# Performance work log

Hardware: AMD Instinct MI355X
Metric: run time of the kernel (lower is better)

The kernel has to match this reference:

```python
import jax, jax.numpy as jnp
import numpy as np

N_NODES = 50000
N_EDGES = 1600000
N_GRAPHS = 512
HEADS = 4
HEAD_DIM = 32
LAYERS = 3
NEG_SLOPE = 0.2


def setup_inputs() -> dict:
    key = jax.random.key(0)
    ks = jax.random.split(key, 7)
    x = jax.random.normal(ks[0], (N_NODES, 128), dtype=jnp.float32)
    Ws = jax.random.normal(ks[1], (LAYERS, 128, 128), dtype=jnp.float32) * 0.1
    att_src = jax.random.normal(ks[2], (LAYERS, HEADS, HEAD_DIM), dtype=jnp.float32) * 0.1
    att_dst = jax.random.normal(ks[3], (LAYERS, HEADS, HEAD_DIM), dtype=jnp.float32) * 0.1
    biases = jnp.zeros((LAYERS, 128), dtype=jnp.float32)
    edge_index = jax.random.randint(ks[4], (2, N_EDGES), 0, N_NODES, dtype=jnp.int64)
    batch = jnp.sort(jax.random.randint(ks[5], (N_NODES,), 0, N_GRAPHS, dtype=jnp.int64))
    return {"x": x, "Ws": Ws, "att_src": att_src, "att_dst": att_dst,
            "biases": biases, "edge_index": edge_index, "batch": batch}


def _gat_layer(x, W, a_s, a_d, b, src, dst, n):
    # linear transform -> per-head features [N, H, C]
    h = (x @ W).reshape(n, HEADS, HEAD_DIM)
    # per-node attention halves [N, H]
    alpha_src = jnp.einsum('nhc,hc->nh', h, a_s)
    alpha_dst = jnp.einsum('nhc,hc->nh', h, a_d)
    # edge logits [E, H]
    e = jax.nn.leaky_relu(alpha_src[src] + alpha_dst[dst], NEG_SLOPE)
    # segment softmax over incoming edges of each destination node
    m = jax.ops.segment_max(e, dst, num_segments=n)
    w = jnp.exp(e - m[dst])
    denom = jax.ops.segment_sum(w, dst, num_segments=n)
    alpha = w / (denom[dst] + 1e-16)
    # weighted scatter-add of source features [E, H, C] -> [N, H, C]
    msg = h[src] * alpha[:, :, None]
    out = jax.ops.segment_sum(msg, dst, num_segments=n)
    return out.reshape(n, HEADS * HEAD_DIM) + b


def reference(x, Ws, att_src, att_dst, biases, edge_index, batch):
    n = x.shape[0]
    # PyG GATConv adds self-loops by default
    loops = jnp.arange(n, dtype=edge_index.dtype)
    src = jnp.concatenate([edge_index[0], loops])
    dst = jnp.concatenate([edge_index[1], loops])
    for l in range(LAYERS):
        x = jax.nn.elu(_gat_layer(x, Ws[l], att_src[l], att_dst[l], biases[l], src, dst, n))
        # dropout is identity in eval mode
    # global mean pool over graphs
    sums = jax.ops.segment_sum(x, batch, num_segments=N_GRAPHS)
    cnt = jax.ops.segment_sum(jnp.ones((n,), x.dtype), batch, num_segments=N_GRAPHS)
    return sums / jnp.maximum(cnt, 1.0)[:, None]
```

## Files before the change

### kernel.cpp

```cpp
#include <hip/hip_runtime.h>
#include <hip/hip_fp16.h>
#include <math.h>

#define HEADS 4
#define HDIM 32
#define FD 128
#define NEG 0.2f
#define BCAP 4608
#define CH 8192
#define CHW 128

typedef _Float16 f16x8 __attribute__((ext_vector_type(8)));
typedef float f32x4 __attribute__((ext_vector_type(4)));

__device__ __forceinline__ float lrelu(float x) { return fmaxf(x, NEG * x); }

__global__ __launch_bounds__(256) void k_prep(const float* __restrict__ x,
                                              __half* __restrict__ o, long nF,
                                              const float* __restrict__ W,
                                              const float* __restrict__ att_s,
                                              const float* __restrict__ att_d,
                                              _Float16* __restrict__ W16T,
                                              float* __restrict__ va_s,
                                              float* __restrict__ va_d,
                                              int* __restrict__ bcnt, int nbuck,
                                              int ncvt) {
    int b = blockIdx.x;
    if (b < ncvt) {
        long i = ((long)b * 256 + threadIdx.x) * 4;
        if (i < nF) {
            float4 v = *(const float4*)&x[i];
            *(__half2*)&o[i] = __floats2half2_rn(v.x, v.y);
            *(__half2*)&o[i + 2] = __floats2half2_rn(v.z, v.w);
        }
        return;
    }
    if (b == ncvt + 3) {
        for (int i = threadIdx.x; i < nbuck; i += 256) bcnt[i] = 0;
        return;
    }
    int l = b - ncvt;
    const float* Wl = W + (long)l * FD * FD;
    _Float16* ow = W16T + (long)l * FD * FD;
    for (int i = threadIdx.x; i < FD * FD; i += 256) {
        int k = i >> 7, n = i & 127;
        ow[n * FD + k] = (_Float16)Wl[i];
    }
    const float* as_l = att_s + l * HEADS * HDIM;
    const float* ad_l = att_d + l * HEADS * HDIM;
    for (int idx = threadIdx.x; idx < HEADS * FD; idx += 256) {
        int hd = idx >> 7, k = idx & 127;
        float ss = 0.f, dd = 0.f;
        for (int c = 0; c < HDIM; ++c) {
            float w = Wl[k * FD + hd * HDIM + c];
            ss += w * as_l[hd * HDIM + c];
            dd += w * ad_l[hd * HDIM + c];
        }
        va_s[(long)l * HEADS * FD + idx] = ss;
        va_d[(long)l * HEADS * FD + idx] = dd;
    }
}

__global__ __launch_bounds__(256) void k_gemm_mfma(const __half* __restrict__ x16,
                                                   const _Float16* __restrict__ W16T,
                                                   __half* __restrict__ h, int N) {
    __shared__ _Float16 wl[FD * FD];
    int t = threadIdx.x;
    for (int i = t * 8; i < FD * FD; i += 2048)
        *(f16x8*)&wl[i] = *(const f16x8*)&W16T[i];

    int w = t >> 6, lane = t & 63;
    int m = lane & 15, quad = lane >> 4;
    int row0 = blockIdx.x * 128 + w * 32;

    f16x8 a[2][4];
    f16x8 zf = {};
#pragma unroll
    for (int rt = 0; rt < 2; ++rt) {
        int gr = row0 + rt * 16 + m;
#pragma unroll
        for (int kc = 0; kc < 4; ++kc)
            a[rt][kc] = (gr < N) ? *(const f16x8*)&x16[(long)gr * FD + kc * 32 + quad * 8] : zf;
    }
    f32x4 acc[2][8];
#pragma unroll
    for (int rt = 0; rt < 2; ++rt)
#pragma unroll
        for (int c = 0; c < 8; ++c) acc[rt][c] = (f32x4){0.f, 0.f, 0.f, 0.f};

    __syncthreads();
#pragma unroll
    for (int c = 0; c < 8; ++c) {
        int nb = c * 16 + m;
#pragma unroll
        for (int kc = 0; kc < 4; ++kc) {
            f16x8 b = *(f16x8*)&wl[nb * FD + kc * 32 + quad * 8];
            acc[0][c] = __builtin_amdgcn_mfma_f32_16x16x32_f16(a[0][kc], b, acc[0][c], 0, 0, 0);
            acc[1][c] = __builtin_amdgcn_mfma_f32_16x16x32_f16(a[1][kc], b, acc[1][c], 0, 0, 0);
        }
    }
#pragma unroll
    for (int rt = 0; rt < 2; ++rt) {
        int rbase = row0 + rt * 16 + quad * 4;
#pragma unroll
        for (int c = 0; c < 8; ++c) {
            int col = c * 16 + m;
#pragma unroll
            for (int i = 0; i < 4; ++i) {
                int gr = rbase + i;
                if (gr < N) h[(long)gr * FD + col] = __float2half(acc[rt][c][i]);
            }
        }
    }
}

__global__ __launch_bounds__(256) void k_alpha(const __half* __restrict__ h,
                                               const float* __restrict__ a_s,
                                               const float* __restrict__ a_d,
                                               float* __restrict__ as_o,
                                               float* __restrict__ ad_o, int N) {
    int t = threadIdx.x;
    int n = blockIdx.x * 16 + (t >> 4);
    if (n >= N) return;
    int c16 = t & 15, gh = c16 >> 2, cb = c16 * 8;
    int c32 = (c16 & 3) * 8;
    float4 raw = *(const float4*)&h[(long)n * FD + cb];
    const __half* hh = (const __half*)&raw;
    float vs = 0.f, vd = 0.f;
#pragma unroll
    for (int i = 0; i < 8; ++i) {
        float hv = __half2float(hh[i]);
        vs += hv * a_s[gh * HDIM + c32 + i];
        vd += hv * a_d[gh * HDIM + c32 + i];
    }
    vs += __shfl_xor(vs, 1); vs += __shfl_xor(vs, 2);
    vd += __shfl_xor(vd, 1); vd += __shfl_xor(vd, 2);
    if ((c16 & 3) == 0) {
        as_o[n * HEADS + gh] = vs;
        ad_o[n * HEADS + gh] = vd;
    }
}

__global__ __launch_bounds__(1024) void k_bin(const int* __restrict__ ei, int NE,
                                              int nbuck,
                                              int* __restrict__ bcnt,
                                              int* __restrict__ binned) {
    __shared__ int hist[512];
    __shared__ int gbase[512];
    int t = threadIdx.x;
    int c0 = blockIdx.x * CH;
    if (t < 512) hist[t] = 0;
    __syncthreads();
    int sub[8], val[8], loff[8];
#pragma unroll
    for (int k = 0; k < 8; ++k) {
        int idx = c0 + k * 1024 + t;
        sub[k] = -1;
        if (idx < NE) {
            int s = ei[idx], d = ei[NE + idx];
            sub[k] = d >> 7;
            val[k] = s | ((d & 127) << 16);
            loff[k] = atomicAdd(&hist[sub[k]], 1);
        }
    }
    __syncthreads();
    if (t < 512 && t < nbuck && hist[t] > 0)
        gbase[t] = atomicAdd(&bcnt[t], hist[t]);
    __syncthreads();
#pragma unroll
    for (int k = 0; k < 8; ++k) {
        if (sub[k] >= 0) {
            int p = gbase[sub[k]] + loff[k];
            if (p < BCAP) binned[(long)sub[k] * BCAP + p] = val[k];
        }
    }
}

__global__ __launch_bounds__(1024) void k_scan_sub(const int* __restrict__ bcnt,
                                                   int* __restrict__ bbase, int n,
                                                   int* __restrict__ rowstart, int N, int NE,
                                                   float* __restrict__ cnt, int G,
                                                   float* __restrict__ outz) {
    __shared__ int sm[1024];
    int t = threadIdx.x;
    int c0 = t * 4;
    int v0 = (c0 < n) ? bcnt[c0] : 0;
    int v1 = (c0 + 1 < n) ? bcnt[c0 + 1] : 0;
    int v2 = (c0 + 2 < n) ? bcnt[c0 + 2] : 0;
    int v3 = (c0 + 3 < n) ? bcnt[c0 + 3] : 0;
    int tot = v0 + v1 + v2 + v3;
    sm[t] = tot;
    if (t < G) cnt[t] = 0.f;
    __syncthreads();
    for (int off = 1; off < 1024; off <<= 1) {
        int u = (t >= off) ? sm[t - off] : 0;
        __syncthreads();
        sm[t] += u;
        __syncthreads();
    }
    int base = sm[t] - tot;
    if (c0 < n) bbase[c0] = base;
    if (c0 + 1 < n) bbase[c0 + 1] = base + v0;
    if (c0 + 2 < n) bbase[c0 + 2] = base + v0 + v1;
    if (c0 + 3 < n) bbase[c0 + 3] = base + v0 + v1 + v2;
    if (t == 1023) {
        bbase[n] = sm[1023];
        rowstart[N] = NE;
    }
    long tot_out = (long)G * FD;
    for (long i = t * 4; i < tot_out; i += 4096)
        *(float4*)&outz[i] = (float4){0.f, 0.f, 0.f, 0.f};
}

__global__ __launch_bounds__(256) void k_bucket_csr(const int* __restrict__ binned,
                                                    const int* __restrict__ bcnt,
                                                    const int* __restrict__ bbase,
                                                    int* __restrict__ csr_src,
                                                    int* __restrict__ rowstart, int N) {
    int b = blockIdx.x;
    int t = threadIdx.x;
    __shared__ int ldeg[128], lofs[128], lcur[128];
    __shared__ int lcsr[BCAP];
    if (t < 128) ldeg[t] = 0;
    __syncthreads();
    int cnt = bcnt[b];
    if (cnt > BCAP) cnt = BCAP;
    int base = bbase[b];
    const int* reg = binned + (long)b * BCAP;
    for (int i = t; i < cnt; i += 256)
        atomicAdd(&ldeg[reg[i] >> 16], 1);
    __syncthreads();
    if (t < 128) lofs[t] = ldeg[t];
    __syncthreads();
    for (int off = 1; off < 128; off <<= 1) {
        int u = (t < 128 && t >= off) ? lofs[t - off] : 0;
        __syncthreads();
        if (t < 128) lofs[t] += u;
        __syncthreads();
    }
    if (t < 128) lcur[t] = lofs[t] - ldeg[t];
    __syncthreads();
    for (int i = t; i < cnt; i += 256) {
        int v = reg[i];
        int p = atomicAdd(&lcur[v >> 16], 1);
        lcsr[p] = v & 0xFFFF;
    }
    __syncthreads();
    for (int i = t; i < cnt; i += 256) csr_src[base + i] = lcsr[i];
    if (t < 128) {
        int d = b * 128 + t;
        if (d < N) rowstart[d] = base + lofs[t] - ldeg[t];
    }
}

__global__ __launch_bounds__(256) void k_aggr(const int* __restrict__ csr_src,
                                              const int* __restrict__ rowstart,
                                              const float* __restrict__ as_,
                                              const float* __restrict__ ad_,
                                              const __half* __restrict__ h,
                                              const float* __restrict__ bias,
                                              const float* __restrict__ va_s,
                                              const float* __restrict__ va_d,
                                              float* __restrict__ as_n,
                                              float* __restrict__ ad_n,
                                              __half* __restrict__ out, int N) {
    __shared__ int s_all[4][CHW];
    int t = threadIdx.x;
    int wv = t >> 6, lane = t & 63;
    int n = blockIdx.x * 4 + wv;
    if (n >= N) return;
    int* s_lds = s_all[wv];
    int c16 = lane & 15, rg = lane >> 4;
    int gh = c16 >> 2;
    int cb = c16 * 8;
    int beg = rowstart[n], end = rowstart[n + 1];
    int deg = end - beg;
    float adn = ad_[n * HEADS + gh];
    float l = 0.f;
    float acc[8] = {0.f, 0.f, 0.f, 0.f, 0.f, 0.f, 0.f, 0.f};

    for (int c0 = 0; c0 < deg; c0 += CHW) {
        int cnt = deg - c0;
        if (cnt > CHW) cnt = CHW;
        for (int i = lane; i < cnt; i += 64) s_lds[i] = csr_src[beg + c0 + i] << 2;
        __builtin_amdgcn_wave_barrier();
#pragma unroll 2
        for (int e = rg; e < cnt; e += 4) {
            int s4 = s_lds[e];
            float lg = lrelu(as_[s4 + gh] + adn);
            float w = __expf(fminf(lg, 30.f));
            l += w;
            float4 raw = *(const float4*)&h[((long)s4 << 5) + cb];
            const __half* hh = (const __half*)&raw;
#pragma unroll
            for (int i = 0; i < 8; ++i)
                acc[i] += __half2float(hh[i]) * w;
        }
        __builtin_amdgcn_wave_barrier();
    }
    l += __shfl_xor(l, 16);
    l += __shfl_xor(l, 32);
#pragma unroll
    for (int i = 0; i < 8; ++i) {
        acc[i] += __shfl_xor(acc[i], 16);
        acc[i] += __shfl_xor(acc[i], 32);
    }
    float sl = lrelu(as_[n * HEADS + gh] + adn);
    float sw = __expf(fminf(sl, 30.f));
    float inv = 1.f / (l + sw + 1e-16f);
    float4 rawh = *(const float4*)&h[(long)n * FD + cb];
    const __half* hh = (const __half*)&rawh;
    float4 b0 = *(const float4*)&bias[cb];
    float4 b1 = *(const float4*)&bias[cb + 4];
    float bb[8] = {b0.x, b0.y, b0.z, b0.w, b1.x, b1.y, b1.z, b1.w};
    float v[8];
#pragma unroll
    for (int i = 0; i < 8; ++i) {
        float u = (acc[i] + sw * __half2float(hh[i])) * inv + bb[i];
        v[i] = u > 0.f ? u : __expf(u) - 1.f;
    }
    if (rg == 0) {
        __half o8[8];
#pragma unroll
        for (int i = 0; i < 8; ++i) o8[i] = __float2half(v[i]);
        *(float4*)&out[(long)n * FD + cb] = *(float4*)o8;
    }
    if (va_s) {
        const float* vs = va_s + rg * FD + cb;
        const float* vd = va_d + rg * FD + cb;
        float ps = 0.f, pd = 0.f;
#pragma unroll
        for (int i = 0; i < 8; ++i) {
            ps += v[i] * vs[i];
            pd += v[i] * vd[i];
        }
        for (int off = 1; off < 16; off <<= 1) {
            ps += __shfl_xor(ps, off);
            pd += __shfl_xor(pd, off);
        }
        if (c16 == 0) {
            as_n[n * HEADS + rg] = ps;
            ad_n[n * HEADS + rg] = pd;
        }
    }
}

__global__ __launch_bounds__(128) void k_pool(const __half* __restrict__ x,
                                              const int* __restrict__ batch,
                                              float* __restrict__ out,
                                              float* __restrict__ cnt, int N) {
    int n0 = blockIdx.x * 32;
    if (n0 >= N) return;
    int n1 = n0 + 32;
    if (n1 > N) n1 = N;
    int ch = threadIdx.x;
    __shared__ int gb[32];
    if (ch < n1 - n0) gb[ch] = batch[n0 + ch];
    __syncthreads();
    int g = gb[0];
    float sum = 0.f, c_local = 0.f;
    for (int n = n0; n < n1; ++n) {
        int gn = gb[n - n0];
        if (gn != g) {
            atomicAdd(&out[(long)g * FD + ch], sum);
            if (ch == 0) atomicAdd(&cnt[g], c_local);
            sum = 0.f;
            c_local = 0.f;
            g = gn;
        }
        sum += __half2float(x[(long)n * FD + ch]);
        c_local += 1.f;
    }
    atomicAdd(&out[(long)g * FD + ch], sum);
    if (ch == 0) atomicAdd(&cnt[g], c_local);
}

__global__ void k_div(float* __restrict__ out, const float* __restrict__ cnt, int G) {
    int i = blockIdx.x * 256 + threadIdx.x;
    if (i >= G * FD) return;
    float c = cnt[i >> 7];
    out[i] /= (c > 1.f ? c : 1.f);
}

extern "C" void kernel_launch(void* const* d_in, const int* in_sizes, int n_in,
                              void* d_out, int out_size, void* d_ws, size_t ws_size,
                              hipStream_t stream) {
    const float* x0     = (const float*)d_in[0];
    const float* Wall   = (const float*)d_in[1];
    const float* att_s  = (const float*)d_in[2];
    const float* att_d  = (const float*)d_in[3];
    const float* biases = (const float*)d_in[4];
    const int*   ei     = (const int*)d_in[5];
    const int*   batch  = (const int*)d_in[6];
    float*       out    = (float*)d_out;

    int N  = in_sizes[0] / FD;
    int NE = in_sizes[5] / 2;
    int G  = out_size / FD;

    int nbuck = (N + 127) >> 7;

    long nF = (long)N * FD;
    float*    wsf      = (float*)d_ws;
    float*    asA      = wsf;
    float*    adA      = asA + (long)N * HEADS;
    float*    asB      = adA + (long)N * HEADS;
    float*    adB      = asB + (long)N * HEADS;
    float*    cnt      = adB + (long)N * HEADS;
    float*    va_s     = cnt + G;
    float*    va_d     = va_s + 3 * HEADS * FD;
    int*      rowstart = (int*)(va_d + 3 * HEADS * FD);
    int*      bcnt     = rowstart + N + 1;
    int*      bbase    = bcnt + nbuck;
    int*      csr_src  = bbase + nbuck + 1;
    __half*   h        = (__half*)(csr_src + NE);
    __half*   x16      = h + nF;
    _Float16* W16T     = (_Float16*)(x16 + nF);
    int*      binned   = (int*)(W16T + 3 * FD * FD);

    int ncvt = (int)((nF / 4 + 255) / 256);

    k_prep<<<ncvt + 4, 256, 0, stream>>>(x0, x16, nF, Wall, att_s, att_d,
                                         W16T, va_s, va_d, bcnt, nbuck, ncvt);
    k_bin<<<(NE + CH - 1) / CH, 1024, 0, stream>>>(ei, NE, nbuck, bcnt, binned);
    k_scan_sub<<<1, 1024, 0, stream>>>(bcnt, bbase, nbuck, rowstart, N, NE, cnt, G, out);
    k_bucket_csr<<<nbuck, 256, 0, stream>>>(binned, bcnt, bbase, csr_src, rowstart, N);

    float* asR[3] = {asA, asB, asA};
    float* adR[3] = {adA, adB, adA};
    for (int l = 0; l < 3; ++l) {
        k_gemm_mfma<<<(N + 127) / 128, 256, 0, stream>>>(x16, W16T + (long)l * FD * FD, h, N);
        if (l == 0)
            k_alpha<<<(N + 15) / 16, 256, 0, stream>>>(h, att_s, att_d, asA, adA, N);
        const float* vs = (l < 2) ? va_s + (long)(l + 1) * HEADS * FD : nullptr;
        const float* vd = (l < 2) ? va_d + (long)(l + 1) * HEADS * FD : nullptr;
        k_aggr<<<(N + 3) / 4, 256, 0, stream>>>(csr_src, rowstart, asR[l], adR[l], h,
                                                biases + l * FD, vs, vd,
                                                asR[l + 1 < 3 ? l + 1 : 0],
                                                adR[l + 1 < 3 ? l + 1 : 0], x16, N);
    }

    k_pool<<<(N + 31) / 32, 128, 0, stream>>>(x16, batch, out, cnt, N);
    k_div<<<(G * FD + 255) / 256, 256, 0, stream>>>(out, cnt, G);
}
```

Before: 356.4 us.

## Split GAT aggregation per head with 16-bit CSR indices and per-layer alpha kernel

Rewrites the aggregation kernel so each block handles one head for 16 nodes, with 16 lanes per node gathering 32-channel head slices over 4 edges at a time. Blocks are ordered so that all four heads of neighbouring node groups run close together, which should help reuse of gathered rows in L2. CSR source indices are stored as 16-bit values, and the LDS index staging is removed. The fused next-layer attention projection is dropped and k_alpha runs every layer instead, which adds a kernel launch and an extra read of h per layer in exchange for a lighter aggregation epilogue. The 16-bit indices only work while the node count stays below 65536.

```diff
diff --git a/kernel.cpp b/kernel.cpp
--- a/kernel.cpp
+++ b/kernel.cpp
@@ -8,7 +8,6 @@
 #define NEG 0.2f
 #define BCAP 4608
 #define CH 8192
-#define CHW 128
 
 typedef _Float16 f16x8 __attribute__((ext_vector_type(8)));
 typedef float f32x4 __attribute__((ext_vector_type(4)));
@@ -18,11 +17,7 @@
 __global__ __launch_bounds__(256) void k_prep(const float* __restrict__ x,
                                               __half* __restrict__ o, long nF,
                                               const float* __restrict__ W,
-                                              const float* __restrict__ att_s,
-                                              const float* __restrict__ att_d,
                                               _Float16* __restrict__ W16T,
-                                              float* __restrict__ va_s,
-                                              float* __restrict__ va_d,
                                               int* __restrict__ bcnt, int nbuck,
                                               int ncvt) {
     int b = blockIdx.x;
@@ -46,19 +41,6 @@
         int k = i >> 7, n = i & 127;
         ow[n * FD + k] = (_Float16)Wl[i];
     }
-    const float* as_l = att_s + l * HEADS * HDIM;
-    const float* ad_l = att_d + l * HEADS * HDIM;
-    for (int idx = threadIdx.x; idx < HEADS * FD; idx += 256) {
-        int hd = idx >> 7, k = idx & 127;
-        float ss = 0.f, dd = 0.f;
-        for (int c = 0; c < HDIM; ++c) {
-            float w = Wl[k * FD + hd * HDIM + c];
-            ss += w * as_l[hd * HDIM + c];
-            dd += w * ad_l[hd * HDIM + c];
-        }
-        va_s[(long)l * HEADS * FD + idx] = ss;
-        va_d[(long)l * HEADS * FD + idx] = dd;
-    }
 }
 
 __global__ __launch_bounds__(256) void k_gemm_mfma(const __half* __restrict__ x16,
@@ -215,7 +197,7 @@
 __global__ __launch_bounds__(256) void k_bucket_csr(const int* __restrict__ binned,
                                                     const int* __restrict__ bcnt,
                                                     const int* __restrict__ bbase,
-                                                    int* __restrict__ csr_src,
+                                                    unsigned short* __restrict__ csr16,
                                                     int* __restrict__ rowstart, int N) {
     int b = blockIdx.x;
     int t = threadIdx.x;
@@ -246,102 +228,76 @@
         lcsr[p] = v & 0xFFFF;
     }
     __syncthreads();
-    for (int i = t; i < cnt; i += 256) csr_src[base + i] = lcsr[i];
+    for (int i = t; i < cnt; i += 256) csr16[base + i] = (unsigned short)lcsr[i];
     if (t < 128) {
         int d = b * 128 + t;
         if (d < N) rowstart[d] = base + lofs[t] - ldeg[t];
     }
 }
 
-__global__ __launch_bounds__(256) void k_aggr(const int* __restrict__ csr_src,
+__global__ __launch_bounds__(256) void k_aggr(const unsigned short* __restrict__ csr16,
                                               const int* __restrict__ rowstart,
                                               const float* __restrict__ as_,
                                               const float* __restrict__ ad_,
                                               const __half* __restrict__ h,
                                               const float* __restrict__ bias,
-                                              const float* __restrict__ va_s,
-                                              const float* __restrict__ va_d,
-                                              float* __restrict__ as_n,
-                                              float* __restrict__ ad_n,
                                               __half* __restrict__ out, int N) {
-    __shared__ int s_all[4][CHW];
     int t = threadIdx.x;
     int wv = t >> 6, lane = t & 63;
-    int n = blockIdx.x * 4 + wv;
-    if (n >= N) return;
-    int* s_lds = s_all[wv];
-    int c16 = lane & 15, rg = lane >> 4;
-    int gh = c16 >> 2;
-    int cb = c16 * 8;
-    int beg = rowstart[n], end = rowstart[n + 1];
-    int deg = end - beg;
-    float adn = ad_[n * HEADS + gh];
+    int b = blockIdx.x;
+    int head = (b & 7) >> 1;
+    int ng = (b >> 3) * 2 + (b & 1);
+    int m = lane >> 4;
+    int g = (lane >> 2) & 3;
+    int l4 = lane & 3;
+    int n = ng * 16 + wv * 4 + m;
+    bool nv = n < N;
+    int nc = nv ? n : 0;
+    int beg = rowstart[nc];
+    int deg = nv ? rowstart[nc + 1] - beg : 0;
+    int hofs = head * 32 + l4 * 8;
+    float adn = ad_[nc * HEADS + head];
+    float asn = as_[nc * HEADS + head];
+    float4 rawh = *(const float4*)&h[(long)nc * FD + hofs];
+    float4 b0 = *(const float4*)&bias[hofs];
+    float4 b1 = *(const float4*)&bias[hofs + 4];
+
     float l = 0.f;
     float acc[8] = {0.f, 0.f, 0.f, 0.f, 0.f, 0.f, 0.f, 0.f};
-
-    for (int c0 = 0; c0 < deg; c0 += CHW) {
-        int cnt = deg - c0;
-        if (cnt > CHW) cnt = CHW;
-        for (int i = lane; i < cnt; i += 64) s_lds[i] = csr_src[beg + c0 + i] << 2;
-        __builtin_amdgcn_wave_barrier();
-#pragma unroll 2
-        for (int e = rg; e < cnt; e += 4) {
-            int s4 = s_lds[e];
-            float lg = lrelu(as_[s4 + gh] + adn);
-            float w = __expf(fminf(lg, 30.f));
-            l += w;
-            float4 raw = *(const float4*)&h[((long)s4 << 5) + cb];
-            const __half* hh = (const __half*)&raw;
-#pragma unroll
-            for (int i = 0; i < 8; ++i)
-                acc[i] += __half2float(hh[i]) * w;
-        }
-        __builtin_amdgcn_wave_barrier();
-    }
-    l += __shfl_xor(l, 16);
-    l += __shfl_xor(l, 32);
+    for (int e0 = 0; e0 < deg; e0 += 4) {
+        int e = e0 + g;
+        int ec = e < deg ? e : deg - 1;
+        int src = (int)__builtin_nontemporal_load(&csr16[beg + ec]);
+        float a = as_[src * HEADS + head];
+        float w = __expf(fminf(lrelu(a + adn), 30.f));
+        if (e >= deg) w = 0.f;
+        l += w;
+        float4 rr = *(const float4*)&h[(long)src * FD + hofs];
+        const __half* hh = (const __half*)&rr;
+#pragma unroll
+        for (int i = 0; i < 8; ++i)
+            acc[i] += __half2float(hh[i]) * w;
+    }
+    l += __shfl_xor(l, 4);
+    l += __shfl_xor(l, 8);
 #pragma unroll
     for (int i = 0; i < 8; ++i) {
-        acc[i] += __shfl_xor(acc[i], 16);
-        acc[i] += __shfl_xor(acc[i], 32);
-    }
-    float sl = lrelu(as_[n * HEADS + gh] + adn);
-    float sw = __expf(fminf(sl, 30.f));
+        acc[i] += __shfl_xor(acc[i], 4);
+        acc[i] += __shfl_xor(acc[i], 8);
+    }
+    float sw = __expf(fminf(lrelu(asn + adn), 30.f));
     float inv = 1.f / (l + sw + 1e-16f);
-    float4 rawh = *(const float4*)&h[(long)n * FD + cb];
     const __half* hh = (const __half*)&rawh;
-    float4 b0 = *(const float4*)&bias[cb];
-    float4 b1 = *(const float4*)&bias[cb + 4];
     float bb[8] = {b0.x, b0.y, b0.z, b0.w, b1.x, b1.y, b1.z, b1.w};
-    float v[8];
-#pragma unroll
-    for (int i = 0; i < 8; ++i) {
-        float u = (acc[i] + sw * __half2float(hh[i])) * inv + bb[i];
-        v[i] = u > 0.f ? u : __expf(u) - 1.f;
-    }
-    if (rg == 0) {
+    if (g == 0 && nv) {
         __half o8[8];
 #pragma unroll
-        for (int i = 0; i < 8; ++i) o8[i] = __float2half(v[i]);
-        *(float4*)&out[(long)n * FD + cb] = *(float4*)o8;
-    }
-    if (va_s) {
-        const float* vs = va_s + rg * FD + cb;
-        const float* vd = va_d + rg * FD + cb;
-        float ps = 0.f, pd = 0.f;
-#pragma unroll
         for (int i = 0; i < 8; ++i) {
-            ps += v[i] * vs[i];
-            pd += v[i] * vd[i];
-        }
-        for (int off = 1; off < 16; off <<= 1) {
-            ps += __shfl_xor(ps, off);
-            pd += __shfl_xor(pd, off);
-        }
-        if (c16 == 0) {
-            as_n[n * HEADS + rg] = ps;
-            ad_n[n * HEADS + rg] = pd;
-        }
+            float u = (acc[i] + sw * __half2float(hh[i])) * inv + bb[i];
+            u = u > 0.f ? u : __expf(u) - 1.f;
+            o8[i] = __float2half(u);
+        }
+        __builtin_nontemporal_store(*(f32x4*)o8, (f32x4*)&out[(long)n * FD + hofs]);
     }
 }
 
@@ -404,40 +360,33 @@
     float*    wsf      = (float*)d_ws;
     float*    asA      = wsf;
     float*    adA      = asA + (long)N * HEADS;
-    float*    asB      = adA + (long)N * HEADS;
-    float*    adB      = asB + (long)N * HEADS;
-    float*    cnt      = adB + (long)N * HEADS;
-    float*    va_s     = cnt + G;
-    float*    va_d     = va_s + 3 * HEADS * FD;
-    int*      rowstart = (int*)(va_d + 3 * HEADS * FD);
+    float*    cnt      = adA + (long)N * HEADS;
+    int*      rowstart = (int*)(cnt + G);
     int*      bcnt     = rowstart + N + 1;
     int*      bbase    = bcnt + nbuck;
-    int*      csr_src  = bbase + nbuck + 1;
-    __half*   h        = (__half*)(csr_src + NE);
+    unsigned short* csr16 = (unsigned short*)(bbase + nbuck + 1);
+    char* pal = (char*)(csr16 + NE);
+    pal = (char*)(((size_t)pal + 63) & ~(size_t)63);
+    __half*   h        = (__half*)pal;
     __half*   x16      = h + nF;
     _Float16* W16T     = (_Float16*)(x16 + nF);
     int*      binned   = (int*)(W16T + 3 * FD * FD);
 
     int ncvt = (int)((nF / 4 + 255) / 256);
 
-    k_prep<<<ncvt + 4, 256, 0, stream>>>(x0, x16, nF, Wall, att_s, att_d,
-                                         W16T, va_s, va_d, bcnt, nbuck, ncvt);
+    k_prep<<<ncvt + 4, 256, 0, stream>>>(x0, x16, nF, Wall, W16T, bcnt, nbuck, ncvt);
     k_bin<<<(NE + CH - 1) / CH, 1024, 0, stream>>>(ei, NE, nbuck, bcnt, binned);
     k_scan_sub<<<1, 1024, 0, stream>>>(bcnt, bbase, nbuck, rowstart, N, NE, cnt, G, out);
-    k_bucket_csr<<<nbuck, 256, 0, stream>>>(binned, bcnt, bbase, csr_src, rowstart, N);
-
-    float* asR[3] = {asA, asB, asA};
-    float* adR[3] = {adA, adB, adA};
+    k_bucket_csr<<<nbuck, 256, 0, stream>>>(binned, bcnt, bbase, csr16, rowstart, N);
+
+    int ngrp = (N + 15) >> 4;
+    int grid_aggr = ((ngrp + 1) >> 1) * 8;
     for (int l = 0; l < 3; ++l) {
         k_gemm_mfma<<<(N + 127) / 128, 256, 0, stream>>>(x16, W16T + (long)l * FD * FD, h, N);
-        if (l == 0)
-            k_alpha<<<(N + 15) / 16, 256, 0, stream>>>(h, att_s, att_d, asA, adA, N);
-        const float* vs = (l < 2) ? va_s + (long)(l + 1) * HEADS * FD : nullptr;
-        const float* vd = (l < 2) ? va_d + (long)(l + 1) * HEADS * FD : nullptr;
-        k_aggr<<<(N + 3) / 4, 256, 0, stream>>>(csr_src, rowstart, asR[l], adR[l], h,
-                                                biases + l * FD, vs, vd,
-                                                asR[l + 1 < 3 ? l + 1 : 0],
-                                                adR[l + 1 < 3 ? l + 1 : 0], x16, N);
+        k_alpha<<<(N + 15) / 16, 256, 0, stream>>>(h, att_s + (long)l * HEADS * HDIM,
+                                                   att_d + (long)l * HEADS * HDIM, asA, adA, N);
+        k_aggr<<<grid_aggr, 256, 0, stream>>>(csr16, rowstart, asA, adA, h,
+                                              biases + l * FD, x16, N);
     }
 
     k_pool<<<(N + 31) / 32, 128, 0, stream>>>(x16, batch, out, cnt, N);
```

After: 573.6 us. 61.0% more time.
